# Kernel tuning notes

Measured on AMD Instinct MI355X. Metric: run time of the kernel, lower is better.

Reference implementation:

```python
import jax, jax.numpy as jnp
import numpy as np

LAYERS = 3
DILATION = 2
RES_NORM = 1.0 / np.sqrt(2.0).astype(np.float32)
NEG_SLOPE = 0.2
T, B, D = 256, 128, 1024


def setup_inputs() -> dict:
    key = jax.random.key(0)
    k0, k1, k2, k3, k4 = jax.random.split(key, 5)
    s = 1.0 / np.sqrt(D)  # torch GRUCell default init bound
    x = jax.random.normal(k0, (1, T, B, D), dtype=jnp.float32)
    W_ih = jax.random.uniform(k1, (LAYERS, 3 * D, D), jnp.float32, -s, s)
    W_hh = jax.random.uniform(k2, (LAYERS, 3 * D, D), jnp.float32, -s, s)
    b_ih = jax.random.uniform(k3, (LAYERS, 3 * D), jnp.float32, -s, s)
    b_hh = jax.random.uniform(k4, (LAYERS, 3 * D), jnp.float32, -s, s)
    return {"x": x, "W_ih": W_ih, "W_hh": W_hh, "b_ih": b_ih, "b_hh": b_hh}


def _gru_cell(x, h, W_ih, W_hh, b_ih, b_hh):
    # torch.nn.GRUCell math
    gi = x @ W_ih.T + b_ih  # [B, 3D]
    gh = h @ W_hh.T + b_hh  # [B, 3D]
    i_r, i_z, i_n = jnp.split(gi, 3, axis=-1)
    h_r, h_z, h_n = jnp.split(gh, 3, axis=-1)
    r = jax.nn.sigmoid(i_r + h_r)
    z = jax.nn.sigmoid(i_z + h_z)
    n = jnp.tanh(i_n + r * h_n)
    return (1.0 - z) * n + z * h


def reference(x, W_ih, W_hh, b_ih, b_hh):
    xs = x[0]  # squeeze(0) -> [T, B, D]
    b, d = xs.shape[1], xs.shape[2]
    # dilated hidden buffers: layer l keeps DILATION**l past hiddens (init None -> zeros)
    bufs0 = tuple(jnp.zeros((DILATION ** l, b, d), xs.dtype) for l in range(LAYERS))

    def step(bufs, x_t):
        h_in = x_t
        new_bufs = []
        for l in range(LAYERS):
            h_out = _gru_cell(h_in, bufs[l][0], W_ih[l], W_hh[l], b_ih[l], b_hh[l])
            # append h_out, pop oldest (roll buffer)
            new_bufs.append(jnp.concatenate([bufs[l][1:], h_out[None]], axis=0))
            # layers > 1 -> dilated residual + LeakyReLU(0.2), scaled by 1/sqrt(2)
            h_in = jax.nn.leaky_relu((h_out + h_in) * RES_NORM, negative_slope=NEG_SLOPE)
        return tuple(new_bufs), h_in

    _, outs = jax.lax.scan(step, bufs0, xs)  # outs: [T, B, D]
    return outs[None]  # unsqueeze(0) -> [1, T, B, D]
```

## Files before the change

### kernel.cpp

```cpp
#include <hip/hip_runtime.h>
#include <hip/hip_bf16.h>

#define TT 256
#define D 1024
#define BD (128 * 1024)
#define NWPL 85
#define NWG 256
#define NUSED 255
#define ROWLEN 1048

typedef __attribute__((ext_vector_type(8))) short bf16x8;
typedef __attribute__((ext_vector_type(4))) float f32x4;

__device__ __forceinline__ unsigned short f2bf(float f) {
    __hip_bfloat16 h = __float2bfloat16(f);
    return *reinterpret_cast<unsigned short*>(&h);
}
__device__ __forceinline__ float bf2f(unsigned short u) {
    unsigned v = (unsigned)u << 16;
    return __builtin_bit_cast(float, v);
}

__global__ __launch_bounds__(256) void cvt_f32_bf16(const float* __restrict__ in,
                                                    unsigned short* __restrict__ out, int n) {
    int i = (blockIdx.x * 256 + threadIdx.x) * 8;
    if (i + 8 <= n) {
        float4 a = *(const float4*)(in + i);
        float4 b = *(const float4*)(in + i + 4);
        unsigned short t[8] = { f2bf(a.x), f2bf(a.y), f2bf(a.z), f2bf(a.w),
                                f2bf(b.x), f2bf(b.y), f2bf(b.z), f2bf(b.w) };
        *(uint4*)(out + i) = *(const uint4*)t;
    }
}

#define GLSC16(dst, base, IMM) asm volatile( \
    "global_load_dwordx4 %0, %1, off offset:%2 sc0 sc1" \
    : "=v"(dst) : "v"(base), "i"(IMM))
#define GLSCD(dst, addr) asm volatile( \
    "global_load_dword %0, %1, off sc0 sc1" : "=v"(dst) : "v"(addr))
#define GLSCU(dst, addr) asm volatile( \
    "global_load_ushort %0, %1, off sc0 sc1" : "=v"(dst) : "v"(addr))
#define WAITV(N) { asm volatile("s_waitcnt vmcnt(%0)" :: "i"(N)); \
                   __builtin_amdgcn_sched_barrier(0); }
#define SB __builtin_amdgcn_sched_barrier(0)
#define AGLD(p) __hip_atomic_load((p), __ATOMIC_RELAXED, __HIP_MEMORY_SCOPE_AGENT)
#define AGST(p, v) __hip_atomic_store((p), (v), __ATOMIC_RELAXED, __HIP_MEMORY_SCOPE_AGENT)

__global__ __launch_bounds__(512, 2) void dgru_dataflow(
    const unsigned short* __restrict__ xbf,
    const float* __restrict__ Wih, const float* __restrict__ Whh,
    const float* __restrict__ bih, const float* __restrict__ bhh,
    unsigned short* __restrict__ ring_bf,
    float* __restrict__ ring_f,
    unsigned short* __restrict__ hin_ring,
    float* __restrict__ out,
    unsigned* __restrict__ prog)
{
    __shared__ unsigned short wlds[78 * ROWLEN];

    const int grp = blockIdx.x & 7;
    const int p = 32 * grp + (blockIdx.x >> 3);
    if (p >= NUSED) return;
    const int layer = p / NWPL;
    const int u     = p % NWPL;
    const int ncols = (u < 4) ? 13 : 12;
    const int c0    = u * 12 + (u < 4 ? u : 4);

    const int tid = threadIdx.x;

    {
        const float* w0 = Wih + (size_t)layer * 3 * D * D;
        const float* w1 = Whh + (size_t)layer * 3 * D * D;
        const int nrows = 6 * ncols;
        const int rh   = tid >> 8;
        const int t255 = tid & 255;
        for (int rid = rh; rid < nrows; rid += 2) {
            int m   = rid / (3 * ncols);
            int rem = rid - m * 3 * ncols;
            int g   = rem / ncols;
            int c   = rem - g * ncols;
            const float* src = (m ? w1 : w0) + ((size_t)g * D + c0 + c) * D + t255 * 4;
            float4 v = *(const float4*)src;
            ushort4 o = { f2bf(v.x), f2bf(v.y), f2bf(v.z), f2bf(v.w) };
            *(ushort4*)&wlds[rid * ROWLEN + t255 * 4] = o;
        }
        __syncthreads();
    }

    const int wave = tid >> 6;
    const int lane = tid & 63;
    const int r15  = lane & 15;
    const int kq   = lane >> 4;
    const int kq8  = kq * 8;
    const int c_cl = (r15 < ncols) ? r15 : (ncols - 1);
    const bool cvalid = r15 < ncols;
    const int col  = c0 + c_cl;

    const float bi2 = bih[layer * 3 * D + 2 * D + col];
    const float bh2 = bhh[layer * 3 * D + 2 * D + col];
    const float bs0 = bih[layer * 3 * D + col] + bhh[layer * 3 * D + col];
    const float bs1 = bih[layer * 3 * D + D + col] + bhh[layer * 3 * D + D + col];

    const unsigned short* bp[6];
    #pragma unroll
    for (int mg = 0; mg < 6; ++mg) bp[mg] = wlds + (mg * ncols + c_cl) * ROWLEN;

    const int arow_off = (wave * 16 + r15) * D + kq8;

    const int dil = 1 << layer;

    unsigned* pr0 = prog;
    unsigned* pr1 = prog + 128;
    unsigned* pr2 = prog + 256;
    unsigned* myflag = prog + layer * 128 + u;

    const int j2 = (lane < 21) ? lane + 64 : lane;

    for (int t = 0; t < TT; ++t) {
        int th1, th2, th3; unsigned *a1, *a2, *a3;
        if (layer == 0)      { a1 = pr0; th1 = t;     a2 = pr1; th2 = t - 7; a3 = pr2; th3 = 0;     }
        else if (layer == 1) { a1 = pr0; th1 = t + 1; a2 = pr1; th2 = t - 1; a3 = pr2; th3 = t - 7; }
        else                 { a1 = pr1; th1 = t + 1; a2 = pr2; th2 = t - 3; a3 = pr2; th3 = 0;     }

        if (wave == 0) {
            for (;;) {
                bool ok = true;
                if (th1 > 0) ok = ok && (int)AGLD(a1 + lane) >= th1 && (int)AGLD(a1 + j2) >= th1;
                if (th2 > 0) ok = ok && (int)AGLD(a2 + lane) >= th2 && (int)AGLD(a2 + j2) >= th2;
                if (th3 > 0) ok = ok && (int)AGLD(a3 + lane) >= th3 && (int)AGLD(a3 + j2) >= th3;
                if (__all(ok)) break;
                __builtin_amdgcn_s_sleep(1);
            }
        }
        __syncthreads();

        const unsigned short* hinb = layer ? hin_ring + (size_t)((layer - 1) * 8 + (t & 7)) * BD
                                           : xbf + (size_t)t * BD;
        const int rs = (t + 8 - dil) & 7, wsl = t & 7;
        const unsigned short* hprevb = ring_bf + (size_t)(layer * 8 + rs) * BD;
        const float*  hprevf = ring_f + (size_t)(layer * 8 + rs) * BD;
        float*        houtf  = ring_f + (size_t)(layer * 8 + wsl) * BD;
        unsigned short* houtb = ring_bf + (size_t)(layer * 8 + wsl) * BD;

        const unsigned short* ba_h = hinb + arow_off;
        const unsigned short* ba_p = hprevb + arow_off;

        float hpv[4]; unsigned ru[4];
        {
            #pragma unroll
            for (int q = 0; q < 4; ++q) {
                const int row = wave * 16 + kq * 4 + q;
                const size_t idx = (size_t)row * D + col;
                GLSCD(hpv[q], hprevf + idx);
                GLSCU(ru[q], hinb + idx);
            }
            SB;
        }

        f32x4 acc[2][3] = {};
        bf16x8 A0[8], A1[8], A2[8], A3[8];

#define ISSUE1(Av, KS, SL) { \
        GLSC16(Av[(SL) * 2 + 0], ba_h, (KS) * 64); \
        GLSC16(Av[(SL) * 2 + 1], ba_p, (KS) * 64); }
#define ISSUEG(Av, BASE) { ISSUE1(Av, (BASE) + 0, 0) ISSUE1(Av, (BASE) + 1, 1) \
                           ISSUE1(Av, (BASE) + 2, 2) ISSUE1(Av, (BASE) + 3, 3) \
                           SB; }
#define COMPG(Av, BASE) { _Pragma("unroll") for (int kk = 0; kk < 4; ++kk) { \
        bf16x8 Bv[6]; \
        _Pragma("unroll") for (int mg = 0; mg < 6; ++mg) \
            Bv[mg] = *(const bf16x8*)(bp[mg] + ((BASE) + kk) * 32 + kq8); \
        _Pragma("unroll") for (int g = 0; g < 3; ++g) { \
            acc[0][g] = __builtin_amdgcn_mfma_f32_16x16x32_bf16(Av[kk * 2 + 0], Bv[g],     acc[0][g], 0, 0, 0); \
            acc[1][g] = __builtin_amdgcn_mfma_f32_16x16x32_bf16(Av[kk * 2 + 1], Bv[3 + g], acc[1][g], 0, 0, 0); } } \
        SB; }

        ISSUEG(A0, 0); ISSUEG(A1, 4); ISSUEG(A2, 8); ISSUEG(A3, 12);
        WAITV(24); COMPG(A0, 0);  ISSUEG(A0, 16);
        WAITV(24); COMPG(A1, 4);  ISSUEG(A1, 20);
        WAITV(24); COMPG(A2, 8);  ISSUEG(A2, 24);
        WAITV(24); COMPG(A3, 12); ISSUEG(A3, 28);
        WAITV(24); COMPG(A0, 16);
        WAITV(16); COMPG(A1, 20);
        WAITV(8);  COMPG(A2, 24);
        WAITV(0);  COMPG(A3, 28);

        #pragma unroll
        for (int q = 0; q < 4; ++q) {
            const int row = wave * 16 + kq * 4 + q;
            const size_t idx = (size_t)row * D + col;
            float xr = acc[0][0][q] + acc[1][0][q] + bs0;
            float xz = acc[0][1][q] + acc[1][1][q] + bs1;
            float rg = 1.f / (1.f + __expf(-xr));
            float zg = 1.f / (1.f + __expf(-xz));
            float ng = tanhf(acc[0][2][q] + bi2 + rg * (acc[1][2][q] + bh2));
            float hp = hpv[q];
            float h  = (1.f - zg) * ng + zg * hp;
            float v = (h + bf2f((unsigned short)ru[q])) * 0.70710678f;
            float y = v > 0.f ? v : 0.2f * v;
            if (cvalid) {
                AGST(&houtf[idx], h);
                AGST(&houtb[idx], f2bf(h));
                if (layer == 2) {
                    AGST(&out[(size_t)t * BD + idx], y);
                } else {
                    AGST(&hin_ring[(size_t)(layer * 8 + (t & 7)) * BD + idx], f2bf(y));
                }
            }
        }

        asm volatile("s_waitcnt vmcnt(0)");
        __syncthreads();
        if (tid == 0) {
            __builtin_amdgcn_fence(__ATOMIC_RELEASE, "agent");
            AGST(myflag, (unsigned)(t + 1));
        }
    }
}

extern "C" void kernel_launch(void* const* d_in, const int* in_sizes, int n_in,
                              void* d_out, int out_size, void* d_ws, size_t ws_size,
                              hipStream_t stream) {
    const float* x   = (const float*)d_in[0];
    const float* Wih = (const float*)d_in[1];
    const float* Whh = (const float*)d_in[2];
    const float* bih = (const float*)d_in[3];
    const float* bhh = (const float*)d_in[4];
    float* out = (float*)d_out;

    char* ws = (char*)d_ws;
    size_t off = 0;
    auto alloc = [&](size_t bytes) -> void* {
        void* p = ws + off;
        off += (bytes + 255) & ~(size_t)255;
        return p;
    };

    const int NX = TT * BD;
    unsigned short* xbf = (unsigned short*)alloc((size_t)NX * 2);

    size_t zstart = off;
    unsigned short* ring_bf  = (unsigned short*)alloc((size_t)24 * BD * 2);
    float*          ring_f   = (float*)alloc((size_t)24 * BD * 4);
    unsigned short* hin_ring = (unsigned short*)alloc((size_t)16 * BD * 2);
    unsigned*       prog     = (unsigned*)alloc(2048);
    size_t zbytes = off - zstart;

    cvt_f32_bf16<<<NX / 8 / 256, 256, 0, stream>>>(x, xbf, NX);
    hipMemsetAsync(ws + zstart, 0, zbytes, stream);

    dgru_dataflow<<<NWG, 512, 0, stream>>>(
        xbf, Wih, Whh, bih, bhh,
        ring_bf, ring_f, hin_ring, out,
        prog);
}
```

Measured before the change: 5.768 ms.

## Use full-history buffers and 256-thread blocks with 32-row tiles per wave

```diff
diff --git a/kernel.cpp b/kernel.cpp
--- a/kernel.cpp
+++ b/kernel.cpp
@@ -8,6 +8,7 @@
 #define NWG 256
 #define NUSED 255
 #define ROWLEN 1048
+#define HSLOTS 264
 
 typedef __attribute__((ext_vector_type(8))) short bf16x8;
 typedef __attribute__((ext_vector_type(4))) float f32x4;
@@ -33,26 +34,25 @@
     }
 }
 
+#define SB __builtin_amdgcn_sched_barrier(0)
+#define AGLD(p) __hip_atomic_load((p), __ATOMIC_RELAXED, __HIP_MEMORY_SCOPE_AGENT)
+#define AGST(p, v) __hip_atomic_store((p), (v), __ATOMIC_RELAXED, __HIP_MEMORY_SCOPE_AGENT)
+#define GLSCD(dst, addr) asm volatile( \
+    "global_load_dword %0, %1, off sc0 sc1" : "=v"(dst) : "v"(addr))
 #define GLSC16(dst, base, IMM) asm volatile( \
     "global_load_dwordx4 %0, %1, off offset:%2 sc0 sc1" \
     : "=v"(dst) : "v"(base), "i"(IMM))
-#define GLSCD(dst, addr) asm volatile( \
-    "global_load_dword %0, %1, off sc0 sc1" : "=v"(dst) : "v"(addr))
 #define GLSCU(dst, addr) asm volatile( \
     "global_load_ushort %0, %1, off sc0 sc1" : "=v"(dst) : "v"(addr))
-#define WAITV(N) { asm volatile("s_waitcnt vmcnt(%0)" :: "i"(N)); \
-                   __builtin_amdgcn_sched_barrier(0); }
-#define SB __builtin_amdgcn_sched_barrier(0)
-#define AGLD(p) __hip_atomic_load((p), __ATOMIC_RELAXED, __HIP_MEMORY_SCOPE_AGENT)
-#define AGST(p, v) __hip_atomic_store((p), (v), __ATOMIC_RELAXED, __HIP_MEMORY_SCOPE_AGENT)
-
-__global__ __launch_bounds__(512, 2) void dgru_dataflow(
+#define WAITV(N) { asm volatile("s_waitcnt vmcnt(%0)" :: "i"(N)); SB; }
+
+__global__ __launch_bounds__(256, 1) void dgru_dedup(
     const unsigned short* __restrict__ xbf,
     const float* __restrict__ Wih, const float* __restrict__ Whh,
     const float* __restrict__ bih, const float* __restrict__ bhh,
-    unsigned short* __restrict__ ring_bf,
+    unsigned short* __restrict__ hist,
     float* __restrict__ ring_f,
-    unsigned short* __restrict__ hin_ring,
+    unsigned short* __restrict__ hin_hist,
     float* __restrict__ out,
     unsigned* __restrict__ prog)
 {
@@ -66,27 +66,24 @@
     const int ncols = (u < 4) ? 13 : 12;
     const int c0    = u * 12 + (u < 4 ? u : 4);
 
-    const int tid = threadIdx.x;
-
     {
         const float* w0 = Wih + (size_t)layer * 3 * D * D;
         const float* w1 = Whh + (size_t)layer * 3 * D * D;
         const int nrows = 6 * ncols;
-        const int rh   = tid >> 8;
-        const int t255 = tid & 255;
-        for (int rid = rh; rid < nrows; rid += 2) {
+        for (int rid = 0; rid < nrows; ++rid) {
             int m   = rid / (3 * ncols);
             int rem = rid - m * 3 * ncols;
             int g   = rem / ncols;
             int c   = rem - g * ncols;
-            const float* src = (m ? w1 : w0) + ((size_t)g * D + c0 + c) * D + t255 * 4;
+            const float* src = (m ? w1 : w0) + ((size_t)g * D + c0 + c) * D + threadIdx.x * 4;
             float4 v = *(const float4*)src;
             ushort4 o = { f2bf(v.x), f2bf(v.y), f2bf(v.z), f2bf(v.w) };
-            *(ushort4*)&wlds[rid * ROWLEN + t255 * 4] = o;
-        }
-        __syncthreads();
-    }
-
+            *(ushort4*)&wlds[rid * ROWLEN + threadIdx.x * 4] = o;
+        }
+        __syncthreads();
+    }
+
+    const int tid  = threadIdx.x;
     const int wave = tid >> 6;
     const int lane = tid & 63;
     const int r15  = lane & 15;
@@ -105,15 +102,178 @@
     #pragma unroll
     for (int mg = 0; mg < 6; ++mg) bp[mg] = wlds + (mg * ncols + c_cl) * ROWLEN;
 
-    const int arow_off = (wave * 16 + r15) * D + kq8;
+    const int arow_off0 = (wave * 32 + r15) * D;
+    const int arow_off1 = (wave * 32 + 16 + r15) * D;
 
     const int dil = 1 << layer;
+    unsigned short* hist_l = hist + (size_t)layer * HSLOTS * BD;
+    float* ringf_l = ring_f + (size_t)layer * 8 * BD;
 
     unsigned* pr0 = prog;
     unsigned* pr1 = prog + 128;
     unsigned* pr2 = prog + 256;
     unsigned* myflag = prog + layer * 128 + u;
 
+    const int j2 = (lane < 21) ? lane + 64 : lane;
+
+    for (int t = 0; t < TT; ++t) {
+        int th1, th2; unsigned *a1, *a2;
+        if (layer == 0)      { a1 = pr0; th1 = t;     a2 = pr0; th2 = 0;     }
+        else if (layer == 1) { a1 = pr0; th1 = t + 1; a2 = pr1; th2 = t - 1; }
+        else                 { a1 = pr1; th1 = t + 1; a2 = pr2; th2 = t - 3; }
+
+        if (wave == 0) {
+            for (;;) {
+                bool ok = true;
+                if (th1 > 0) ok = ok && (int)AGLD(a1 + lane) >= th1 && (int)AGLD(a1 + j2) >= th1;
+                if (th2 > 0) ok = ok && (int)AGLD(a2 + lane) >= th2 && (int)AGLD(a2 + j2) >= th2;
+                if (__all(ok)) break;
+                __builtin_amdgcn_s_sleep(1);
+            }
+        }
+        __syncthreads();
+
+        const unsigned short* hinb = layer ? hin_hist + (size_t)((layer - 1) * TT + t) * BD
+                                           : xbf + (size_t)t * BD;
+        const unsigned short* hprevb = hist_l + (size_t)(t - dil + 8) * BD;
+        unsigned short*       houtb  = hist_l + (size_t)(t + 8) * BD;
+        const float* hprevf = ringf_l + (size_t)((t - dil) & 7) * BD;
+        float*       houtf  = ringf_l + (size_t)(t & 7) * BD;
+
+        float hpv[8], rsv[8];
+        #pragma unroll
+        for (int rtl = 0; rtl < 2; ++rtl)
+            #pragma unroll
+            for (int q = 0; q < 4; ++q) {
+                const int row = wave * 32 + rtl * 16 + kq * 4 + q;
+                const size_t idx = (size_t)row * D + col;
+                GLSCD(hpv[rtl * 4 + q], hprevf + idx);
+                rsv[rtl * 4 + q] = bf2f(hinb[idx]);
+            }
+        SB;
+
+        f32x4 acc[2][2][3] = {};
+        bf16x8 A0[16], A1[16], A2[16];
+
+#define ISSUE1(Av, KS, SL) { \
+        Av[(SL) * 4 + 0] = *(const bf16x8*)(hinb   + arow_off0 + (KS) * 32 + kq8); \
+        Av[(SL) * 4 + 1] = *(const bf16x8*)(hprevb + arow_off0 + (KS) * 32 + kq8); \
+        Av[(SL) * 4 + 2] = *(const bf16x8*)(hinb   + arow_off1 + (KS) * 32 + kq8); \
+        Av[(SL) * 4 + 3] = *(const bf16x8*)(hprevb + arow_off1 + (KS) * 32 + kq8); }
+#define ISSUEG(Av, BASE) { ISSUE1(Av, (BASE) + 0, 0) ISSUE1(Av, (BASE) + 1, 1) \
+                           ISSUE1(Av, (BASE) + 2, 2) ISSUE1(Av, (BASE) + 3, 3) \
+                           SB; }
+#define COMPG(Av, BASE) { _Pragma("unroll") for (int kk = 0; kk < 4; ++kk) { \
+        bf16x8 Bv[6]; \
+        _Pragma("unroll") for (int mg = 0; mg < 6; ++mg) \
+            Bv[mg] = *(const bf16x8*)(bp[mg] + ((BASE) + kk) * 32 + kq8); \
+        _Pragma("unroll") for (int g = 0; g < 3; ++g) { \
+            acc[0][0][g] = __builtin_amdgcn_mfma_f32_16x16x32_bf16(Av[kk * 4 + 0], Bv[g],     acc[0][0][g], 0, 0, 0); \
+            acc[0][1][g] = __builtin_amdgcn_mfma_f32_16x16x32_bf16(Av[kk * 4 + 1], Bv[3 + g], acc[0][1][g], 0, 0, 0); \
+            acc[1][0][g] = __builtin_amdgcn_mfma_f32_16x16x32_bf16(Av[kk * 4 + 2], Bv[g],     acc[1][0][g], 0, 0, 0); \
+            acc[1][1][g] = __builtin_amdgcn_mfma_f32_16x16x32_bf16(Av[kk * 4 + 3], Bv[3 + g], acc[1][1][g], 0, 0, 0); } } \
+        SB; }
+
+        ISSUEG(A0, 0);  ISSUEG(A1, 4);  ISSUEG(A2, 8);
+        COMPG(A0, 0);   ISSUEG(A0, 12);
+        COMPG(A1, 4);   ISSUEG(A1, 16);
+        COMPG(A2, 8);   ISSUEG(A2, 20);
+        COMPG(A0, 12);  ISSUEG(A0, 24);
+        COMPG(A1, 16);  ISSUEG(A1, 28);
+        COMPG(A2, 20);
+        COMPG(A0, 24);
+        COMPG(A1, 28);
+
+        asm volatile("s_waitcnt vmcnt(0)");
+        SB;
+
+        #pragma unroll
+        for (int rtl = 0; rtl < 2; ++rtl) {
+            #pragma unroll
+            for (int q = 0; q < 4; ++q) {
+                const int row = wave * 32 + rtl * 16 + kq * 4 + q;
+                const size_t idx = (size_t)row * D + col;
+                float xr = acc[rtl][0][0][q] + acc[rtl][1][0][q] + bs0;
+                float xz = acc[rtl][0][1][q] + acc[rtl][1][1][q] + bs1;
+                float rg = 1.f / (1.f + __expf(-xr));
+                float zg = 1.f / (1.f + __expf(-xz));
+                float ng = tanhf(acc[rtl][0][2][q] + bi2 + rg * (acc[rtl][1][2][q] + bh2));
+                float hp = hpv[rtl * 4 + q];
+                float h  = (1.f - zg) * ng + zg * hp;
+                float v = (h + rsv[rtl * 4 + q]) * 0.70710678f;
+                float y = v > 0.f ? v : 0.2f * v;
+                if (cvalid) {
+                    AGST(&houtf[idx], h);
+                    AGST(&houtb[idx], f2bf(h));
+                    if (layer == 2) {
+                        AGST(&out[(size_t)t * BD + idx], y);
+                    } else {
+                        AGST(&hin_hist[(size_t)(layer * TT + t) * BD + idx], f2bf(y));
+                    }
+                }
+            }
+        }
+
+        asm volatile("s_waitcnt vmcnt(0)");
+        __syncthreads();
+        if (tid == 0) {
+            __builtin_amdgcn_fence(__ATOMIC_RELEASE, "agent");
+            AGST(myflag, (unsigned)(t + 1));
+        }
+    }
+}
+
+__global__ __launch_bounds__(512, 2) void dgru_mall(
+    const unsigned short* __restrict__ xbf,
+    const float* __restrict__ Wih, const float* __restrict__ Whh,
+    const float* __restrict__ bih, const float* __restrict__ bhh,
+    unsigned short* __restrict__ ring_bf, float* __restrict__ ring_f,
+    unsigned short* __restrict__ hin_ring, float* __restrict__ out,
+    unsigned* __restrict__ prog)
+{
+    __shared__ unsigned short wlds[78 * ROWLEN];
+    const int grp = blockIdx.x & 7;
+    const int p = 32 * grp + (blockIdx.x >> 3);
+    if (p >= NUSED) return;
+    const int layer = p / NWPL;
+    const int u     = p % NWPL;
+    const int ncols = (u < 4) ? 13 : 12;
+    const int c0    = u * 12 + (u < 4 ? u : 4);
+    const int tid = threadIdx.x;
+    {
+        const float* w0 = Wih + (size_t)layer * 3 * D * D;
+        const float* w1 = Whh + (size_t)layer * 3 * D * D;
+        const int nrows = 6 * ncols;
+        const int rh = tid >> 8, t255 = tid & 255;
+        for (int rid = rh; rid < nrows; rid += 2) {
+            int m = rid / (3 * ncols);
+            int rem = rid - m * 3 * ncols;
+            int g = rem / ncols, c = rem - g * ncols;
+            const float* src = (m ? w1 : w0) + ((size_t)g * D + c0 + c) * D + t255 * 4;
+            float4 v = *(const float4*)src;
+            ushort4 o = { f2bf(v.x), f2bf(v.y), f2bf(v.z), f2bf(v.w) };
+            *(ushort4*)&wlds[rid * ROWLEN + t255 * 4] = o;
+        }
+        __syncthreads();
+    }
+    const int wave = tid >> 6, lane = tid & 63;
+    const int r15 = lane & 15, kq = lane >> 4, kq8 = kq * 8;
+    const int c_cl = (r15 < ncols) ? r15 : (ncols - 1);
+    const bool cvalid = r15 < ncols;
+    const int col = c0 + c_cl;
+    const float bi2 = bih[layer * 3 * D + 2 * D + col];
+    const float bh2 = bhh[layer * 3 * D + 2 * D + col];
+    const float bs0 = bih[layer * 3 * D + col] + bhh[layer * 3 * D + col];
+    const float bs1 = bih[layer * 3 * D + D + col] + bhh[layer * 3 * D + D + col];
+    const unsigned short* bp[6];
+    #pragma unroll
+    for (int mg = 0; mg < 6; ++mg) bp[mg] = wlds + (mg * ncols + c_cl) * ROWLEN;
+    const int arow_off = (wave * 16 + r15) * D + kq8;
+    const int dil = 1 << layer;
+    unsigned* pr0 = prog;
+    unsigned* pr1 = prog + 128;
+    unsigned* pr2 = prog + 256;
+    unsigned* myflag = prog + layer * 128 + u;
     const int j2 = (lane < 21) ? lane + 64 : lane;
 
     for (int t = 0; t < TT; ++t) {
@@ -121,7 +281,6 @@
         if (layer == 0)      { a1 = pr0; th1 = t;     a2 = pr1; th2 = t - 7; a3 = pr2; th3 = 0;     }
         else if (layer == 1) { a1 = pr0; th1 = t + 1; a2 = pr1; th2 = t - 1; a3 = pr2; th3 = t - 7; }
         else                 { a1 = pr1; th1 = t + 1; a2 = pr2; th2 = t - 3; a3 = pr2; th3 = 0;     }
-
         if (wave == 0) {
             for (;;) {
                 bool ok = true;
@@ -133,40 +292,32 @@
             }
         }
         __syncthreads();
-
         const unsigned short* hinb = layer ? hin_ring + (size_t)((layer - 1) * 8 + (t & 7)) * BD
                                            : xbf + (size_t)t * BD;
         const int rs = (t + 8 - dil) & 7, wsl = t & 7;
         const unsigned short* hprevb = ring_bf + (size_t)(layer * 8 + rs) * BD;
-        const float*  hprevf = ring_f + (size_t)(layer * 8 + rs) * BD;
-        float*        houtf  = ring_f + (size_t)(layer * 8 + wsl) * BD;
+        const float* hprevf = ring_f + (size_t)(layer * 8 + rs) * BD;
+        float* houtf = ring_f + (size_t)(layer * 8 + wsl) * BD;
         unsigned short* houtb = ring_bf + (size_t)(layer * 8 + wsl) * BD;
-
         const unsigned short* ba_h = hinb + arow_off;
         const unsigned short* ba_p = hprevb + arow_off;
-
         float hpv[4]; unsigned ru[4];
-        {
-            #pragma unroll
-            for (int q = 0; q < 4; ++q) {
-                const int row = wave * 16 + kq * 4 + q;
-                const size_t idx = (size_t)row * D + col;
-                GLSCD(hpv[q], hprevf + idx);
-                GLSCU(ru[q], hinb + idx);
-            }
-            SB;
-        }
-
+        #pragma unroll
+        for (int q = 0; q < 4; ++q) {
+            const int row = wave * 16 + kq * 4 + q;
+            const size_t idx = (size_t)row * D + col;
+            GLSCD(hpv[q], hprevf + idx);
+            GLSCU(ru[q], hinb + idx);
+        }
+        SB;
         f32x4 acc[2][3] = {};
         bf16x8 A0[8], A1[8], A2[8], A3[8];
-
-#define ISSUE1(Av, KS, SL) { \
+#define FISSUE1(Av, KS, SL) { \
         GLSC16(Av[(SL) * 2 + 0], ba_h, (KS) * 64); \
         GLSC16(Av[(SL) * 2 + 1], ba_p, (KS) * 64); }
-#define ISSUEG(Av, BASE) { ISSUE1(Av, (BASE) + 0, 0) ISSUE1(Av, (BASE) + 1, 1) \
-                           ISSUE1(Av, (BASE) + 2, 2) ISSUE1(Av, (BASE) + 3, 3) \
-                           SB; }
-#define COMPG(Av, BASE) { _Pragma("unroll") for (int kk = 0; kk < 4; ++kk) { \
+#define FISSUEG(Av, BASE) { FISSUE1(Av, (BASE) + 0, 0) FISSUE1(Av, (BASE) + 1, 1) \
+                            FISSUE1(Av, (BASE) + 2, 2) FISSUE1(Av, (BASE) + 3, 3) SB; }
+#define FCOMPG(Av, BASE) { _Pragma("unroll") for (int kk = 0; kk < 4; ++kk) { \
         bf16x8 Bv[6]; \
         _Pragma("unroll") for (int mg = 0; mg < 6; ++mg) \
             Bv[mg] = *(const bf16x8*)(bp[mg] + ((BASE) + kk) * 32 + kq8); \
@@ -174,17 +325,15 @@
             acc[0][g] = __builtin_amdgcn_mfma_f32_16x16x32_bf16(Av[kk * 2 + 0], Bv[g],     acc[0][g], 0, 0, 0); \
             acc[1][g] = __builtin_amdgcn_mfma_f32_16x16x32_bf16(Av[kk * 2 + 1], Bv[3 + g], acc[1][g], 0, 0, 0); } } \
         SB; }
-
-        ISSUEG(A0, 0); ISSUEG(A1, 4); ISSUEG(A2, 8); ISSUEG(A3, 12);
-        WAITV(24); COMPG(A0, 0);  ISSUEG(A0, 16);
-        WAITV(24); COMPG(A1, 4);  ISSUEG(A1, 20);
-        WAITV(24); COMPG(A2, 8);  ISSUEG(A2, 24);
-        WAITV(24); COMPG(A3, 12); ISSUEG(A3, 28);
-        WAITV(24); COMPG(A0, 16);
-        WAITV(16); COMPG(A1, 20);
-        WAITV(8);  COMPG(A2, 24);
-        WAITV(0);  COMPG(A3, 28);
-
+        FISSUEG(A0, 0); FISSUEG(A1, 4); FISSUEG(A2, 8); FISSUEG(A3, 12);
+        WAITV(24); FCOMPG(A0, 0);  FISSUEG(A0, 16);
+        WAITV(24); FCOMPG(A1, 4);  FISSUEG(A1, 20);
+        WAITV(24); FCOMPG(A2, 8);  FISSUEG(A2, 24);
+        WAITV(24); FCOMPG(A3, 12); FISSUEG(A3, 28);
+        WAITV(24); FCOMPG(A0, 16);
+        WAITV(16); FCOMPG(A1, 20);
+        WAITV(8);  FCOMPG(A2, 24);
+        WAITV(0);  FCOMPG(A3, 28);
         #pragma unroll
         for (int q = 0; q < 4; ++q) {
             const int row = wave * 16 + kq * 4 + q;
@@ -194,21 +343,16 @@
             float rg = 1.f / (1.f + __expf(-xr));
             float zg = 1.f / (1.f + __expf(-xz));
             float ng = tanhf(acc[0][2][q] + bi2 + rg * (acc[1][2][q] + bh2));
-            float hp = hpv[q];
-            float h  = (1.f - zg) * ng + zg * hp;
+            float h = (1.f - zg) * ng + zg * hpv[q];
             float v = (h + bf2f((unsigned short)ru[q])) * 0.70710678f;
             float y = v > 0.f ? v : 0.2f * v;
             if (cvalid) {
                 AGST(&houtf[idx], h);
                 AGST(&houtb[idx], f2bf(h));
-                if (layer == 2) {
-                    AGST(&out[(size_t)t * BD + idx], y);
-                } else {
-                    AGST(&hin_ring[(size_t)(layer * 8 + (t & 7)) * BD + idx], f2bf(y));
-                }
+                if (layer == 2) AGST(&out[(size_t)t * BD + idx], y);
+                else            AGST(&hin_ring[(size_t)(layer * 8 + (t & 7)) * BD + idx], f2bf(y));
             }
         }
-
         asm volatile("s_waitcnt vmcnt(0)");
         __syncthreads();
         if (tid == 0) {
@@ -239,18 +383,35 @@
     const int NX = TT * BD;
     unsigned short* xbf = (unsigned short*)alloc((size_t)NX * 2);
 
-    size_t zstart = off;
-    unsigned short* ring_bf  = (unsigned short*)alloc((size_t)24 * BD * 2);
-    float*          ring_f   = (float*)alloc((size_t)24 * BD * 4);
-    unsigned short* hin_ring = (unsigned short*)alloc((size_t)16 * BD * 2);
-    unsigned*       prog     = (unsigned*)alloc(2048);
-    size_t zbytes = off - zstart;
-
-    cvt_f32_bf16<<<NX / 8 / 256, 256, 0, stream>>>(x, xbf, NX);
-    hipMemsetAsync(ws + zstart, 0, zbytes, stream);
-
-    dgru_dataflow<<<NWG, 512, 0, stream>>>(
-        xbf, Wih, Whh, bih, bhh,
-        ring_bf, ring_f, hin_ring, out,
-        prog);
-}
+    const size_t NEED = ((size_t)NX * 2) + ((size_t)3 * HSLOTS * BD * 2)
+                      + ((size_t)24 * BD * 4) + ((size_t)2 * TT * BD * 2) + 65536;
+
+    if (ws_size >= NEED) {
+        unsigned short* hist     = (unsigned short*)alloc((size_t)3 * HSLOTS * BD * 2);
+        float*          ring_f   = (float*)alloc((size_t)24 * BD * 4);
+        unsigned short* hin_hist = (unsigned short*)alloc((size_t)2 * TT * BD * 2);
+        unsigned*       prog     = (unsigned*)alloc(2048);
+
+        cvt_f32_bf16<<<NX / 8 / 256, 256, 0, stream>>>(x, xbf, NX);
+        for (int l = 0; l < 3; ++l)
+            hipMemsetAsync(hist + (size_t)l * HSLOTS * BD, 0, (size_t)8 * BD * 2, stream);
+        hipMemsetAsync(ring_f, 0, (size_t)24 * BD * 4, stream);
+        hipMemsetAsync(prog, 0, 2048, stream);
+
+        dgru_dedup<<<NWG, 256, 0, stream>>>(
+            xbf, Wih, Whh, bih, bhh, hist, ring_f, hin_hist, out, prog);
+    } else {
+        size_t zstart = off;
+        unsigned short* ring_bf  = (unsigned short*)alloc((size_t)24 * BD * 2);
+        float*          ring_f   = (float*)alloc((size_t)24 * BD * 4);
+        unsigned short* hin_ring = (unsigned short*)alloc((size_t)16 * BD * 2);
+        unsigned*       prog     = (unsigned*)alloc(2048);
+        size_t zbytes = off - zstart;
+
+        cvt_f32_bf16<<<NX / 8 / 256, 256, 0, stream>>>(x, xbf, NX);
+        hipMemsetAsync(ws + zstart, 0, zbytes, stream);
+
+        dgru_mall<<<NWG, 512, 0, stream>>>(
+            xbf, Wih, Whh, bih, bhh, ring_bf, ring_f, hin_ring, out, prog);
+    }
+}
```

After: 5.868 ms. No clear change (+1.7%).
